# Kernel optimization log

Hardware: AMD Instinct MI355X
Metric: run time of the kernel (lower is better)

Reference implementation:

```python
import jax, jax.numpy as jnp
import numpy as np

EMBED_DIM = 1024
NUM_HEADS = 16
HEAD_DIM = EMBED_DIM // NUM_HEADS


def setup_inputs() -> dict:
    key = jax.random.key(0)
    ks = jax.random.split(key, 5)
    scale = 1.0 / np.sqrt(EMBED_DIM)
    x = jax.random.normal(ks[0], (2, 2048, EMBED_DIM), dtype=jnp.float32)
    W_qkv = jax.random.uniform(ks[1], (EMBED_DIM, 3 * EMBED_DIM), jnp.float32, -scale, scale)
    b_qkv = jax.random.uniform(ks[2], (3 * EMBED_DIM,), jnp.float32, -scale, scale)
    W_out = jax.random.uniform(ks[3], (EMBED_DIM, EMBED_DIM), jnp.float32, -scale, scale)
    b_out = jax.random.uniform(ks[4], (EMBED_DIM,), jnp.float32, -scale, scale)
    return {"x": x, "W_qkv": W_qkv, "b_qkv": b_qkv, "W_out": W_out, "b_out": b_out}


def reference(x, W_qkv, b_qkv, W_out, b_out):
    B, T, C = x.shape
    H, D = NUM_HEADS, HEAD_DIM
    qkv = x @ W_qkv + b_qkv                       # [B,T,3C]
    q, k, v = jnp.split(qkv, 3, axis=-1)
    # [B,T,C] -> [B,H,T,D]
    q = q.reshape(B, T, H, D).transpose(0, 2, 1, 3)
    k = k.reshape(B, T, H, D).transpose(0, 2, 1, 3)
    v = v.reshape(B, T, H, D).transpose(0, 2, 1, 3)
    scores = jnp.einsum('bhqd,bhkd->bhqk', q, k) / np.sqrt(D)
    attn = jax.nn.softmax(scores, axis=-1)
    out = jnp.einsum('bhqk,bhkd->bhqd', attn, v)  # [B,H,T,D]
    out = out.transpose(0, 2, 1, 3).reshape(B, T, C)
    return out @ W_out + b_out
```

## Files before the change

kernel.cpp:

```cpp
#include <hip/hip_runtime.h>
#include <hip/hip_bf16.h>

#define TB 2048
#define CC 1024
#define HH 16
#define DD 64
#define MM 4096
#define N3 3072
#define KVB 64
#define NT (TB / KVB)

typedef __bf16 bf16x8 __attribute__((ext_vector_type(8)));
typedef float f32x4 __attribute__((ext_vector_type(4)));
typedef unsigned short ushort8 __attribute__((ext_vector_type(8)));
typedef unsigned short u16;

#define QSCALE 0.180336880693612f

__device__ __forceinline__ u16 f2b(float f) {
    unsigned int x = __float_as_uint(f);
    x = (x + 0x7fffu + ((x >> 16) & 1u)) >> 16;
    return (u16)x;
}

__device__ __forceinline__ unsigned cvt_pk_bf16(float lo, float hi) {
    unsigned r;
    asm("v_cvt_pk_bf16_f32 %0, %1, %2" : "=v"(r) : "v"(lo), "v"(hi));
    return r;
}

__device__ __forceinline__ void gld16(const u16* g, u16* l) {
    __builtin_amdgcn_global_load_lds(
        (const __attribute__((address_space(1))) unsigned int*)g,
        (__attribute__((address_space(3))) unsigned int*)l, 16, 0, 0);
}

__global__ __launch_bounds__(256) void cvt_bf16(const float* __restrict__ in,
                                                u16* __restrict__ out, int n) {
    int i = (blockIdx.x * 256 + threadIdx.x) * 4;
    if (i >= n) return;
    float4 v = *reinterpret_cast<const float4*>(in + i);
    union { u16 u[4]; uint2 v2; } r;
    r.u[0] = f2b(v.x); r.u[1] = f2b(v.y); r.u[2] = f2b(v.z); r.u[3] = f2b(v.w);
    *reinterpret_cast<uint2*>(out + i) = r.v2;
}

__global__ __launch_bounds__(256) void transpose_cvt2(const float* __restrict__ wqkv,
                                                      u16* __restrict__ wqkvT,
                                                      const float* __restrict__ wout,
                                                      u16* __restrict__ woutT) {
    __shared__ float tl[64][65];
    const int bx = blockIdx.x;
    const float* in; u16* out; int N, n0;
    if (bx < 48) { in = wqkv; out = wqkvT; N = 3072; n0 = bx * 64; }
    else         { in = wout; out = woutT; N = 1024; n0 = (bx - 48) * 64; }
    const int k0 = blockIdx.y * 64;
    const int tid = threadIdx.x;
#pragma unroll
    for (int rep = 0; rep < 16; ++rep) {
        int idx = rep * 256 + tid;
        int r = idx >> 6, c = idx & 63;
        tl[r][c] = in[(size_t)(k0 + r) * N + n0 + c];
    }
    __syncthreads();
#pragma unroll
    for (int rep = 0; rep < 16; ++rep) {
        int idx = rep * 256 + tid;
        int r = idx >> 6, c = idx & 63;
        out[(size_t)(n0 + r) * 1024 + k0 + c] = f2b(tl[c][r]);
    }
}

__global__ __launch_bounds__(256) void gemm_qkv(const u16* __restrict__ xb,
                                                const u16* __restrict__ wT,
                                                const float* __restrict__ bias,
                                                u16* __restrict__ qg,
                                                u16* __restrict__ kg,
                                                u16* __restrict__ vtg) {
    __shared__ u16 smem[2 * 128 * 64];
    u16* As = smem;
    u16* Bs = smem + 128 * 64;
    const int m0 = blockIdx.y * 128, n0 = blockIdx.x * 128;
    const int tid = threadIdx.x;
    const int w = tid >> 6, lane = tid & 63, lr = lane & 15, h = lane >> 4;
    const int wr = w >> 1, wc = w & 1;
    f32x4 acc[4][4] = {};

    for (int k0 = 0; k0 < 1024; k0 += 64) {
        __syncthreads();
#pragma unroll
        for (int j = 0; j < 4; ++j) {
            int L = j * 256 + tid;
            int r = L >> 3, c = L & 7;
            int csw = (c ^ (r & 7)) << 3;
            gld16(xb + (size_t)(m0 + r) * 1024 + k0 + csw, As + L * 8);
            gld16(wT + (size_t)(n0 + r) * 1024 + k0 + csw, Bs + L * 8);
        }
        __syncthreads();
#pragma unroll
        for (int kk = 0; kk < 2; ++kk) {
            bf16x8 a[4], b[4];
            int cc = kk * 4 + h;
#pragma unroll
            for (int m = 0; m < 4; ++m) {
                int R = wr * 64 + m * 16 + lr;
                a[m] = *reinterpret_cast<const bf16x8*>((const char*)As + R * 128 + ((cc ^ (R & 7)) << 4));
            }
#pragma unroll
            for (int n = 0; n < 4; ++n) {
                int R = wc * 64 + n * 16 + lr;
                b[n] = *reinterpret_cast<const bf16x8*>((const char*)Bs + R * 128 + ((cc ^ (R & 7)) << 4));
            }
#pragma unroll
            for (int m = 0; m < 4; ++m)
#pragma unroll
                for (int n = 0; n < 4; ++n)
                    acc[m][n] = __builtin_amdgcn_mfma_f32_16x16x32_bf16(a[m], b[n], acc[m][n], 0, 0, 0);
        }
    }

    const int nthird = n0 >> 10;
    if (nthird == 2) {
        __syncthreads();
#pragma unroll
        for (int n = 0; n < 4; ++n) {
            int nloc = wc * 64 + n * 16 + lr;
            unsigned xorv = (unsigned)(nloc & 15) << 4;
            float bv = bias[n0 + nloc];
#pragma unroll
            for (int m = 0; m < 4; ++m) {
                int mloc = wr * 64 + m * 16 + h * 4;
                int mp = (mloc & ~31) | (((mloc >> 2) & 3) << 3) | (((mloc >> 4) & 1) << 2);
                union { u16 u[4]; unsigned long long ll; } pk4;
#pragma unroll
                for (int reg = 0; reg < 4; ++reg)
                    pk4.u[reg] = f2b(acc[m][n][reg] + bv);
                *reinterpret_cast<unsigned long long*>(
                    (char*)smem + nloc * 256 + ((unsigned)(mp * 2) ^ xorv)) = pk4.ll;
            }
        }
        __syncthreads();
        const int b = m0 >> 11, t0 = m0 & 2047;
        const int c16 = tid & 15;
#pragma unroll
        for (int step = 0; step < 8; ++step) {
            int row = (tid >> 4) + step * 16;
            ushort8 vch = *reinterpret_cast<const ushort8*>(
                (const char*)smem + row * 256 + ((unsigned)((c16 ^ (row & 15)) << 4)));
            int c1 = (n0 + row) & 1023;
            int hh = c1 >> 6, dd = c1 & 63;
            *reinterpret_cast<ushort8*>(
                vtg + ((size_t)(b * HH + hh) * DD + dd) * TB + t0 + c16 * 8) = vch;
        }
    } else {
#pragma unroll
        for (int n = 0; n < 4; ++n) {
            int ng = n0 + wc * 64 + n * 16 + lr;
            int c1 = ng & 1023;
            int hh = c1 >> 6, dd = c1 & 63;
            float bv = bias[ng];
#pragma unroll
            for (int m = 0; m < 4; ++m) {
#pragma unroll
                for (int reg = 0; reg < 4; ++reg) {
                    int mg = m0 + wr * 64 + m * 16 + h * 4 + reg;
                    int b = mg >> 11, t = mg & 2047;
                    size_t bh = (size_t)b * HH + hh;
                    float val = acc[m][n][reg] + bv;
                    if (nthird == 0) qg[(bh * TB + t) * DD + dd] = f2b(val * QSCALE);
                    else             kg[(bh * TB + t) * DD + dd] = f2b(val);
                }
            }
        }
    }
}

__global__ __launch_bounds__(512, 4) void attn(const u16* __restrict__ qg,
                                               const u16* __restrict__ kg,
                                               const u16* __restrict__ vtg,
                                               u16* __restrict__ ao) {
    __shared__ u16 Kt[2][KVB * 64];
    __shared__ u16 Vt[2][64 * KVB];
    const int bh = blockIdx.y;
    const int q0 = blockIdx.x * 128;
    const int tid = threadIdx.x, w = tid >> 6, lane = tid & 63;
    const int lr = lane & 15, h = lane >> 4;
    const u16* qb = qg + (size_t)bh * TB * DD;
    const u16* kb = kg + (size_t)bh * TB * DD;
    const u16* vb = vtg + (size_t)bh * DD * TB;

#define STAGE(buf, kbase) do {                                                          \
    int rk = tid >> 3, ck = tid & 7;                                                    \
    int csw = (ck ^ (rk & 7)) << 3;                                                     \
    gld16(kb + (size_t)((kbase) + rk) * DD + csw, Kt[buf] + tid * 8);                   \
    gld16(vb + (size_t)rk * TB + (kbase) + csw, Vt[buf] + tid * 8);                     \
} while (0)

    bf16x8 bq[2];
#pragma unroll
    for (int kk = 0; kk < 2; ++kk)
        bq[kk] = *reinterpret_cast<const bf16x8*>(qb + (size_t)(q0 + w * 16 + lr) * DD + kk * 32 + h * 8);

    f32x4 o[4] = {};
    float m_r = -1e30f;
    float l_r = 0.f;

    STAGE(0, 0);
    __syncthreads();
    int cur = 0;

    for (int kt = 0; kt < NT; ++kt) {
        if (kt < NT - 1) STAGE(cur ^ 1, (kt + 1) * KVB);
        const u16* ktc = Kt[cur];
        const u16* vtc = Vt[cur];

        f32x4 s[4] = {};
        __builtin_amdgcn_s_setprio(1);
#pragma unroll
        for (int kk = 0; kk < 2; ++kk) {
            int cc = kk * 4 + h;
#pragma unroll
            for (int ng = 0; ng < 4; ++ng) {
                int R = ng * 16 + lr;
                bf16x8 ak = *reinterpret_cast<const bf16x8*>((const char*)ktc + R * 128 + ((cc ^ (R & 7)) << 4));
                s[ng] = __builtin_amdgcn_mfma_f32_16x16x32_bf16(ak, bq[kk], s[ng], 0, 0, 0);
            }
        }
        __builtin_amdgcn_s_setprio(0);

        float tmx[4];
#pragma unroll
        for (int ng = 0; ng < 4; ++ng)
            tmx[ng] = fmaxf(fmaxf(s[ng][0], s[ng][1]), fmaxf(s[ng][2], s[ng][3]));
        float pm = fmaxf(fmaxf(tmx[0], tmx[1]), fmaxf(tmx[2], tmx[3]));
        pm = fmaxf(pm, __shfl_xor(pm, 16));
        pm = fmaxf(pm, __shfl_xor(pm, 32));

        if (!__all(pm - m_r <= 8.0f)) {
            float mn = fmaxf(m_r, pm);
            float fr = __builtin_amdgcn_exp2f(m_r - mn);
            m_r = mn;
            l_r *= fr;
#pragma unroll
            for (int reg = 0; reg < 4; ++reg) {
                float fro = __shfl(fr, h * 4 + reg);
#pragma unroll
                for (int ngd = 0; ngd < 4; ++ngd)
                    o[ngd][reg] *= fro;
            }
        }

        float ps[4];
#pragma unroll
        for (int ng = 0; ng < 4; ++ng) {
            s[ng][0] = __builtin_amdgcn_exp2f(s[ng][0] - m_r);
            s[ng][1] = __builtin_amdgcn_exp2f(s[ng][1] - m_r);
            s[ng][2] = __builtin_amdgcn_exp2f(s[ng][2] - m_r);
            s[ng][3] = __builtin_amdgcn_exp2f(s[ng][3] - m_r);
            ps[ng] = (s[ng][0] + s[ng][1]) + (s[ng][2] + s[ng][3]);
        }
        float sum = (ps[0] + ps[1]) + (ps[2] + ps[3]);
        sum += __shfl_xor(sum, 16);
        sum += __shfl_xor(sum, 32);
        l_r += sum;

        __builtin_amdgcn_s_setprio(1);
#pragma unroll
        for (int kk = 0; kk < 2; ++kk) {
            union { unsigned u[4]; bf16x8 v; } ap;
            ap.u[0] = cvt_pk_bf16(s[2 * kk][0], s[2 * kk][1]);
            ap.u[1] = cvt_pk_bf16(s[2 * kk][2], s[2 * kk][3]);
            ap.u[2] = cvt_pk_bf16(s[2 * kk + 1][0], s[2 * kk + 1][1]);
            ap.u[3] = cvt_pk_bf16(s[2 * kk + 1][2], s[2 * kk + 1][3]);
            int cpos = kk * 4 + h;
#pragma unroll
            for (int ngd = 0; ngd < 4; ++ngd) {
                int d = ngd * 16 + lr;
                bf16x8 bv = *reinterpret_cast<const bf16x8*>((const char*)vtc + d * 128 + ((cpos ^ (d & 7)) << 4));
                o[ngd] = __builtin_amdgcn_mfma_f32_16x16x32_bf16(ap.v, bv, o[ngd], 0, 0, 0);
            }
        }
        __builtin_amdgcn_s_setprio(0);
        __syncthreads();
        cur ^= 1;
    }
#undef STAGE

    float linv[4];
#pragma unroll
    for (int reg = 0; reg < 4; ++reg)
        linv[reg] = 1.0f / __shfl(l_r, h * 4 + reg);

    const int b = bh >> 4, hh = bh & 15;
#pragma unroll
    for (int ngd = 0; ngd < 4; ++ngd) {
#pragma unroll
        for (int reg = 0; reg < 4; ++reg) {
            int t = q0 + w * 16 + h * 4 + reg;
            int col = hh * DD + ngd * 16 + lr;
            ao[((size_t)(b * TB + t)) * CC + col] = f2b(o[ngd][reg] * linv[reg]);
        }
    }
}

__global__ __launch_bounds__(256) void gemm_out(const u16* __restrict__ ao,
                                                const u16* __restrict__ wT,
                                                const float* __restrict__ bias,
                                                float* __restrict__ out) {
    __shared__ u16 As[64 * 64];
    __shared__ u16 Bs[128 * 64];
    const int m0 = blockIdx.y * 64, n0 = blockIdx.x * 128;
    const int tid = threadIdx.x;
    const int w = tid >> 6, lane = tid & 63, lr = lane & 15, h = lane >> 4;
    f32x4 acc[4][2] = {};

    for (int k0 = 0; k0 < 1024; k0 += 64) {
        __syncthreads();
#pragma unroll
        for (int j = 0; j < 2; ++j) {
            int L = j * 256 + tid;
            int r = L >> 3, c = L & 7;
            gld16(ao + (size_t)(m0 + r) * 1024 + k0 + ((c ^ (r & 7)) << 3), As + L * 8);
        }
#pragma unroll
        for (int j = 0; j < 4; ++j) {
            int L = j * 256 + tid;
            int r = L >> 3, c = L & 7;
            gld16(wT + (size_t)(n0 + r) * 1024 + k0 + ((c ^ (r & 7)) << 3), Bs + L * 8);
        }
        __syncthreads();
#pragma unroll
        for (int kk = 0; kk < 2; ++kk) {
            bf16x8 a[4], b[2];
            int cc = kk * 4 + h;
#pragma unroll
            for (int m = 0; m < 4; ++m) {
                int R = m * 16 + lr;
                a[m] = *reinterpret_cast<const bf16x8*>((const char*)As + R * 128 + ((cc ^ (R & 7)) << 4));
            }
#pragma unroll
            for (int n = 0; n < 2; ++n) {
                int R = w * 32 + n * 16 + lr;
                b[n] = *reinterpret_cast<const bf16x8*>((const char*)Bs + R * 128 + ((cc ^ (R & 7)) << 4));
            }
#pragma unroll
            for (int m = 0; m < 4; ++m)
#pragma unroll
                for (int n = 0; n < 2; ++n)
                    acc[m][n] = __builtin_amdgcn_mfma_f32_16x16x32_bf16(a[m], b[n], acc[m][n], 0, 0, 0);
        }
    }

#pragma unroll
    for (int n = 0; n < 2; ++n) {
        int ng = n0 + w * 32 + n * 16 + lr;
        float bv = bias[ng];
#pragma unroll
        for (int m = 0; m < 4; ++m) {
#pragma unroll
            for (int reg = 0; reg < 4; ++reg) {
                int mg = m0 + m * 16 + h * 4 + reg;
                out[(size_t)mg * 1024 + ng] = acc[m][n][reg] + bv;
            }
        }
    }
}

extern "C" void kernel_launch(void* const* d_in, const int* in_sizes, int n_in,
                              void* d_out, int out_size, void* d_ws, size_t ws_size,
                              hipStream_t stream) {
    const float* x     = (const float*)d_in[0];
    const float* W_qkv = (const float*)d_in[1];
    const float* b_qkv = (const float*)d_in[2];
    const float* W_out = (const float*)d_in[3];
    const float* b_out = (const float*)d_in[4];
    float* out = (float*)d_out;

    char* ws = (char*)d_ws;
    u16* xb    = (u16*)(ws);
    u16* wqkvT = (u16*)(ws + (size_t)( 8u << 20));
    u16* woutT = (u16*)(ws + (size_t)(14u << 20));
    u16* qg    = (u16*)(ws + (size_t)(16u << 20));
    u16* kg    = (u16*)(ws + (size_t)(24u << 20));
    u16* vtg   = (u16*)(ws + (size_t)(32u << 20));
    u16* ao    = xb;

    hipLaunchKernelGGL(cvt_bf16, dim3(4096), dim3(256), 0, stream, x, xb, MM * CC);
    hipLaunchKernelGGL(transpose_cvt2, dim3(64, 16), dim3(256), 0, stream, W_qkv, wqkvT, W_out, woutT);
    hipLaunchKernelGGL(gemm_qkv, dim3(24, 32), dim3(256), 0, stream, xb, wqkvT, b_qkv, qg, kg, vtg);
    hipLaunchKernelGGL(attn, dim3(16, 32), dim3(512), 0, stream, qg, kg, vtg, ao);
    hipLaunchKernelGGL(gemm_out, dim3(8, 64), dim3(256), 0, stream, ao, woutT, b_out, out);
}
```

Baseline: 125.8 us.

## Process two query row-groups per wave in attention to reuse K/V fragments

The attention kernel moves from 8 waves of 16 query rows each to 4 waves of 32 rows each, keeping two independent softmax states per wave. Each K and V fragment read from LDS now feeds two MFMAs, which halves LDS read traffic per FLOP, and the staging loop is split across fewer threads. In exchange, register pressure roughly doubles for accumulators and scores, and there are fewer waves per block to hide latency.

```diff
diff --git a/kernel.cpp b/kernel.cpp
--- a/kernel.cpp
+++ b/kernel.cpp
@@ -175,7 +175,7 @@
     }
 }
 
-__global__ __launch_bounds__(512, 4) void attn(const u16* __restrict__ qg,
+__global__ __launch_bounds__(256, 2) void attn(const u16* __restrict__ qg,
                                                const u16* __restrict__ kg,
                                                const u16* __restrict__ vtg,
                                                u16* __restrict__ ao) {
@@ -190,20 +190,26 @@
     const u16* vb = vtg + (size_t)bh * DD * TB;
 
 #define STAGE(buf, kbase) do {                                                          \
-    int rk = tid >> 3, ck = tid & 7;                                                    \
-    int csw = (ck ^ (rk & 7)) << 3;                                                     \
-    gld16(kb + (size_t)((kbase) + rk) * DD + csw, Kt[buf] + tid * 8);                   \
-    gld16(vb + (size_t)rk * TB + (kbase) + csw, Vt[buf] + tid * 8);                     \
-} while (0)
-
-    bf16x8 bq[2];
-#pragma unroll
-    for (int kk = 0; kk < 2; ++kk)
-        bq[kk] = *reinterpret_cast<const bf16x8*>(qb + (size_t)(q0 + w * 16 + lr) * DD + kk * 32 + h * 8);
-
-    f32x4 o[4] = {};
-    float m_r = -1e30f;
-    float l_r = 0.f;
+    _Pragma("unroll")                                                                   \
+    for (int j = 0; j < 2; ++j) {                                                       \
+        int L = j * 256 + tid;                                                          \
+        int rk = L >> 3, ck = L & 7;                                                    \
+        int csw = (ck ^ (rk & 7)) << 3;                                                 \
+        gld16(kb + (size_t)((kbase) + rk) * DD + csw, Kt[buf] + L * 8);                 \
+        gld16(vb + (size_t)rk * TB + (kbase) + csw, Vt[buf] + L * 8);                   \
+    } } while (0)
+
+    bf16x8 bq[2][2];
+#pragma unroll
+    for (int g = 0; g < 2; ++g)
+#pragma unroll
+        for (int kk = 0; kk < 2; ++kk)
+            bq[g][kk] = *reinterpret_cast<const bf16x8*>(
+                qb + (size_t)(q0 + w * 32 + g * 16 + lr) * DD + kk * 32 + h * 8);
+
+    f32x4 o[2][4] = {};
+    float m0 = -1e30f, m1 = -1e30f;
+    float l0 = 0.f, l1 = 0.f;
 
     STAGE(0, 0);
     __syncthreads();
@@ -214,7 +220,7 @@
         const u16* ktc = Kt[cur];
         const u16* vtc = Vt[cur];
 
-        f32x4 s[4] = {};
+        f32x4 s[2][4] = {};
         __builtin_amdgcn_s_setprio(1);
 #pragma unroll
         for (int kk = 0; kk < 2; ++kk) {
@@ -222,62 +228,94 @@
 #pragma unroll
             for (int ng = 0; ng < 4; ++ng) {
                 int R = ng * 16 + lr;
-                bf16x8 ak = *reinterpret_cast<const bf16x8*>((const char*)ktc + R * 128 + ((cc ^ (R & 7)) << 4));
-                s[ng] = __builtin_amdgcn_mfma_f32_16x16x32_bf16(ak, bq[kk], s[ng], 0, 0, 0);
+                bf16x8 ak = *reinterpret_cast<const bf16x8*>(
+                    (const char*)ktc + R * 128 + ((cc ^ (R & 7)) << 4));
+                s[0][ng] = __builtin_amdgcn_mfma_f32_16x16x32_bf16(ak, bq[0][kk], s[0][ng], 0, 0, 0);
+                s[1][ng] = __builtin_amdgcn_mfma_f32_16x16x32_bf16(ak, bq[1][kk], s[1][ng], 0, 0, 0);
             }
         }
         __builtin_amdgcn_s_setprio(0);
 
-        float tmx[4];
-#pragma unroll
-        for (int ng = 0; ng < 4; ++ng)
-            tmx[ng] = fmaxf(fmaxf(s[ng][0], s[ng][1]), fmaxf(s[ng][2], s[ng][3]));
-        float pm = fmaxf(fmaxf(tmx[0], tmx[1]), fmaxf(tmx[2], tmx[3]));
-        pm = fmaxf(pm, __shfl_xor(pm, 16));
-        pm = fmaxf(pm, __shfl_xor(pm, 32));
-
-        if (!__all(pm - m_r <= 8.0f)) {
-            float mn = fmaxf(m_r, pm);
-            float fr = __builtin_amdgcn_exp2f(m_r - mn);
-            m_r = mn;
-            l_r *= fr;
+        float pm0, pm1;
+        {
+            float a0 = fmaxf(fmaxf(s[0][0][0], s[0][0][1]), fmaxf(s[0][0][2], s[0][0][3]));
+            float a1 = fmaxf(fmaxf(s[0][1][0], s[0][1][1]), fmaxf(s[0][1][2], s[0][1][3]));
+            float a2 = fmaxf(fmaxf(s[0][2][0], s[0][2][1]), fmaxf(s[0][2][2], s[0][2][3]));
+            float a3 = fmaxf(fmaxf(s[0][3][0], s[0][3][1]), fmaxf(s[0][3][2], s[0][3][3]));
+            pm0 = fmaxf(fmaxf(a0, a1), fmaxf(a2, a3));
+            float b0 = fmaxf(fmaxf(s[1][0][0], s[1][0][1]), fmaxf(s[1][0][2], s[1][0][3]));
+            float b1 = fmaxf(fmaxf(s[1][1][0], s[1][1][1]), fmaxf(s[1][1][2], s[1][1][3]));
+            float b2 = fmaxf(fmaxf(s[1][2][0], s[1][2][1]), fmaxf(s[1][2][2], s[1][2][3]));
+            float b3 = fmaxf(fmaxf(s[1][3][0], s[1][3][1]), fmaxf(s[1][3][2], s[1][3][3]));
+            pm1 = fmaxf(fmaxf(b0, b1), fmaxf(b2, b3));
+        }
+        pm0 = fmaxf(pm0, __shfl_xor(pm0, 16));
+        pm0 = fmaxf(pm0, __shfl_xor(pm0, 32));
+        pm1 = fmaxf(pm1, __shfl_xor(pm1, 16));
+        pm1 = fmaxf(pm1, __shfl_xor(pm1, 32));
+
+        bool need = (pm0 - m0 > 8.0f) || (pm1 - m1 > 8.0f);
+        if (__any(need)) {
+            float mn0 = fmaxf(m0, pm0), mn1 = fmaxf(m1, pm1);
+            float fr0 = __builtin_amdgcn_exp2f(m0 - mn0);
+            float fr1 = __builtin_amdgcn_exp2f(m1 - mn1);
+            m0 = mn0; m1 = mn1;
+            l0 *= fr0; l1 *= fr1;
 #pragma unroll
             for (int reg = 0; reg < 4; ++reg) {
-                float fro = __shfl(fr, h * 4 + reg);
-#pragma unroll
-                for (int ngd = 0; ngd < 4; ++ngd)
-                    o[ngd][reg] *= fro;
-            }
-        }
-
-        float ps[4];
+                float fa = __shfl(fr0, h * 4 + reg);
+                float fb = __shfl(fr1, h * 4 + reg);
+#pragma unroll
+                for (int ngd = 0; ngd < 4; ++ngd) {
+                    o[0][ngd][reg] *= fa;
+                    o[1][ngd][reg] *= fb;
+                }
+            }
+        }
+
+        float ps0[4], ps1[4];
 #pragma unroll
         for (int ng = 0; ng < 4; ++ng) {
-            s[ng][0] = __builtin_amdgcn_exp2f(s[ng][0] - m_r);
-            s[ng][1] = __builtin_amdgcn_exp2f(s[ng][1] - m_r);
-            s[ng][2] = __builtin_amdgcn_exp2f(s[ng][2] - m_r);
-            s[ng][3] = __builtin_amdgcn_exp2f(s[ng][3] - m_r);
-            ps[ng] = (s[ng][0] + s[ng][1]) + (s[ng][2] + s[ng][3]);
-        }
-        float sum = (ps[0] + ps[1]) + (ps[2] + ps[3]);
-        sum += __shfl_xor(sum, 16);
-        sum += __shfl_xor(sum, 32);
-        l_r += sum;
+            s[0][ng][0] = __builtin_amdgcn_exp2f(s[0][ng][0] - m0);
+            s[0][ng][1] = __builtin_amdgcn_exp2f(s[0][ng][1] - m0);
+            s[0][ng][2] = __builtin_amdgcn_exp2f(s[0][ng][2] - m0);
+            s[0][ng][3] = __builtin_amdgcn_exp2f(s[0][ng][3] - m0);
+            ps0[ng] = (s[0][ng][0] + s[0][ng][1]) + (s[0][ng][2] + s[0][ng][3]);
+            s[1][ng][0] = __builtin_amdgcn_exp2f(s[1][ng][0] - m1);
+            s[1][ng][1] = __builtin_amdgcn_exp2f(s[1][ng][1] - m1);
+            s[1][ng][2] = __builtin_amdgcn_exp2f(s[1][ng][2] - m1);
+            s[1][ng][3] = __builtin_amdgcn_exp2f(s[1][ng][3] - m1);
+            ps1[ng] = (s[1][ng][0] + s[1][ng][1]) + (s[1][ng][2] + s[1][ng][3]);
+        }
+        float sum0 = (ps0[0] + ps0[1]) + (ps0[2] + ps0[3]);
+        float sum1 = (ps1[0] + ps1[1]) + (ps1[2] + ps1[3]);
+        sum0 += __shfl_xor(sum0, 16);
+        sum0 += __shfl_xor(sum0, 32);
+        sum1 += __shfl_xor(sum1, 16);
+        sum1 += __shfl_xor(sum1, 32);
+        l0 += sum0;
+        l1 += sum1;
 
         __builtin_amdgcn_s_setprio(1);
 #pragma unroll
         for (int kk = 0; kk < 2; ++kk) {
-            union { unsigned u[4]; bf16x8 v; } ap;
-            ap.u[0] = cvt_pk_bf16(s[2 * kk][0], s[2 * kk][1]);
-            ap.u[1] = cvt_pk_bf16(s[2 * kk][2], s[2 * kk][3]);
-            ap.u[2] = cvt_pk_bf16(s[2 * kk + 1][0], s[2 * kk + 1][1]);
-            ap.u[3] = cvt_pk_bf16(s[2 * kk + 1][2], s[2 * kk + 1][3]);
+            union { unsigned u[4]; bf16x8 v; } ap0, ap1;
+            ap0.u[0] = cvt_pk_bf16(s[0][2 * kk][0], s[0][2 * kk][1]);
+            ap0.u[1] = cvt_pk_bf16(s[0][2 * kk][2], s[0][2 * kk][3]);
+            ap0.u[2] = cvt_pk_bf16(s[0][2 * kk + 1][0], s[0][2 * kk + 1][1]);
+            ap0.u[3] = cvt_pk_bf16(s[0][2 * kk + 1][2], s[0][2 * kk + 1][3]);
+            ap1.u[0] = cvt_pk_bf16(s[1][2 * kk][0], s[1][2 * kk][1]);
+            ap1.u[1] = cvt_pk_bf16(s[1][2 * kk][2], s[1][2 * kk][3]);
+            ap1.u[2] = cvt_pk_bf16(s[1][2 * kk + 1][0], s[1][2 * kk + 1][1]);
+            ap1.u[3] = cvt_pk_bf16(s[1][2 * kk + 1][2], s[1][2 * kk + 1][3]);
             int cpos = kk * 4 + h;
 #pragma unroll
             for (int ngd = 0; ngd < 4; ++ngd) {
                 int d = ngd * 16 + lr;
-                bf16x8 bv = *reinterpret_cast<const bf16x8*>((const char*)vtc + d * 128 + ((cpos ^ (d & 7)) << 4));
-                o[ngd] = __builtin_amdgcn_mfma_f32_16x16x32_bf16(ap.v, bv, o[ngd], 0, 0, 0);
+                bf16x8 bv = *reinterpret_cast<const bf16x8*>(
+                    (const char*)vtc + d * 128 + ((cpos ^ (d & 7)) << 4));
+                o[0][ngd] = __builtin_amdgcn_mfma_f32_16x16x32_bf16(ap0.v, bv, o[0][ngd], 0, 0, 0);
+                o[1][ngd] = __builtin_amdgcn_mfma_f32_16x16x32_bf16(ap1.v, bv, o[1][ngd], 0, 0, 0);
             }
         }
         __builtin_amdgcn_s_setprio(0);
@@ -286,19 +324,23 @@
     }
 #undef STAGE
 
-    float linv[4];
-#pragma unroll
-    for (int reg = 0; reg < 4; ++reg)
-        linv[reg] = 1.0f / __shfl(l_r, h * 4 + reg);
+    float linv0[4], linv1[4];
+#pragma unroll
+    for (int reg = 0; reg < 4; ++reg) {
+        linv0[reg] = 1.0f / __shfl(l0, h * 4 + reg);
+        linv1[reg] = 1.0f / __shfl(l1, h * 4 + reg);
+    }
 
     const int b = bh >> 4, hh = bh & 15;
 #pragma unroll
     for (int ngd = 0; ngd < 4; ++ngd) {
 #pragma unroll
         for (int reg = 0; reg < 4; ++reg) {
-            int t = q0 + w * 16 + h * 4 + reg;
             int col = hh * DD + ngd * 16 + lr;
-            ao[((size_t)(b * TB + t)) * CC + col] = f2b(o[ngd][reg] * linv[reg]);
+            int t0g = q0 + w * 32 + h * 4 + reg;
+            ao[((size_t)(b * TB + t0g)) * CC + col] = f2b(o[0][ngd][reg] * linv0[reg]);
+            int t1g = t0g + 16;
+            ao[((size_t)(b * TB + t1g)) * CC + col] = f2b(o[1][ngd][reg] * linv1[reg]);
         }
     }
 }
@@ -388,6 +430,6 @@
     hipLaunchKernelGGL(cvt_bf16, dim3(4096), dim3(256), 0, stream, x, xb, MM * CC);
     hipLaunchKernelGGL(transpose_cvt2, dim3(64, 16), dim3(256), 0, stream, W_qkv, wqkvT, W_out, woutT);
     hipLaunchKernelGGL(gemm_qkv, dim3(24, 32), dim3(256), 0, stream, xb, wqkvT, b_qkv, qg, kg, vtg);
-    hipLaunchKernelGGL(attn, dim3(16, 32), dim3(512), 0, stream, qg, kg, vtg, ao);
+    hipLaunchKernelGGL(attn, dim3(16, 32), dim3(256), 0, stream, qg, kg, vtg, ao);
     hipLaunchKernelGGL(gemm_out, dim3(8, 64), dim3(256), 0, stream, ao, woutT, b_out, out);
 }
```

New measurement: 129.4 us. 2.9% more time.
